# Kernel optimization log

Hardware: AMD Instinct MI355X
Metric: run time of the kernel (lower is better)

The kernel has to match this reference:

```python
import jax, jax.numpy as jnp
import numpy as np

N, F_IN, HEADS, D_HEAD, NCLASS = 4096, 512, 8, 8, 16
NEG_INF = -9e15
LEAKY_SLOPE = 0.2


def setup_inputs() -> dict:
    key = jax.random.key(0)
    ks = jax.random.split(key, 8)
    x = jax.random.normal(ks[0], (N, F_IN), dtype=jnp.float32)
    adj = (jax.random.uniform(ks[1], (N, N)) < 0.01).astype(jnp.float32)
    adj = jnp.maximum(adj, jnp.eye(N, dtype=jnp.float32))
    s1 = 1.0 / np.sqrt(F_IN)
    s2 = 1.0 / np.sqrt(HEADS * D_HEAD)
    W1 = jax.random.normal(ks[2], (HEADS, F_IN, D_HEAD), dtype=jnp.float32) * s1
    a1_src = jax.random.normal(ks[3], (HEADS, D_HEAD), dtype=jnp.float32)
    a1_dst = jax.random.normal(ks[4], (HEADS, D_HEAD), dtype=jnp.float32)
    W2 = jax.random.normal(ks[5], (1, HEADS * D_HEAD, NCLASS), dtype=jnp.float32) * s2
    a2_src = jax.random.normal(ks[6], (1, NCLASS), dtype=jnp.float32)
    a2_dst = jax.random.normal(ks[7], (1, NCLASS), dtype=jnp.float32)
    return {"x": x, "adj": adj, "W1": W1, "a1_src": a1_src, "a1_dst": a1_dst,
            "W2": W2, "a2_src": a2_src, "a2_dst": a2_dst}


def gat_conv(x, adj, W, a_src, a_dst):
    # x: [N, F]; W: [H, F, D]; a_src/a_dst: [H, D]
    h = jnp.einsum('nf,hfd->hnd', x, W)              # [H, N, D]
    e_src = jnp.einsum('hnd,hd->hn', h, a_src)        # [H, N]
    e_dst = jnp.einsum('hnd,hd->hn', h, a_dst)        # [H, N]
    e = e_src[:, :, None] + e_dst[:, None, :]         # [H, N, N]
    e = jax.nn.leaky_relu(e, LEAKY_SLOPE)
    e = jnp.where(adj[None] > 0, e, NEG_INF)
    att = jax.nn.softmax(e, axis=-1)                  # masked row softmax
    out = jnp.einsum('hnm,hmd->hnd', att, h)          # [H, N, D]
    H, n, d = out.shape
    return jnp.transpose(out, (1, 0, 2)).reshape(n, H * d)  # concat heads


def reference(x, adj, W1, a1_src, a1_dst, W2, a2_src, a2_dst):
    # eval mode: dropout is identity
    h = gat_conv(x, adj, W1, a1_src, a1_dst)          # [N, 64]
    h = jax.nn.elu(h)
    out = gat_conv(h, adj, W2, a2_src, a2_dst)        # [N, NCLASS]
    return jax.nn.log_softmax(out, axis=-1)
```

## Files before the change

### kernel.cpp

```cpp
#include <hip/hip_runtime.h>
#include <math.h>

#define NN 4096
#define F_IN 512
#define HEADS 8
#define D_HEAD 8
#define C1 64
#define NCLASS 16
#define MAX_DEG 128
#define LEAKY 0.2f

__global__ __launch_bounds__(256) void k_proj1(const float* __restrict__ x,
                                               const float* __restrict__ W1,
                                               const float* __restrict__ a1s,
                                               const float* __restrict__ a1d,
                                               float* __restrict__ h1,
                                               float* __restrict__ es1,
                                               float* __restrict__ ed1) {
    __shared__ float xs[16 * 512];
    const int t = threadIdx.x;
    const int n0 = blockIdx.x * 16;
    const float4* x4 = (const float4*)(x + (size_t)n0 * F_IN);
    float4* xs4 = (float4*)xs;
#pragma unroll
    for (int i = 0; i < 8; i++) xs4[t + i * 256] = x4[t + i * 256];
    __syncthreads();

    const int c = t & 63;
    const int h = c >> 3, d = c & 7;
    const int rr = t >> 6;
    const float* wp = W1 + h * (F_IN * D_HEAD) + d;
    const float* xr0 = xs + (rr * 4 + 0) * F_IN;
    const float* xr1 = xs + (rr * 4 + 1) * F_IN;
    const float* xr2 = xs + (rr * 4 + 2) * F_IN;
    const float* xr3 = xs + (rr * 4 + 3) * F_IN;
    float a0 = 0.f, a1 = 0.f, a2 = 0.f, a3 = 0.f;
#pragma unroll 8
    for (int f = 0; f < F_IN; f++) {
        float w = wp[f * 8];
        a0 += xr0[f] * w;
        a1 += xr1[f] * w;
        a2 += xr2[f] * w;
        a3 += xr3[f] * w;
    }
    const float as = a1s[c], ad = a1d[c];
    float accs[4] = {a0, a1, a2, a3};
#pragma unroll
    for (int q = 0; q < 4; q++) {
        int n = n0 + rr * 4 + q;
        float v = accs[q];
        h1[(size_t)n * C1 + c] = v;
        float vs = v * as, vd = v * ad;
        vs += __shfl_xor(vs, 1, 64); vd += __shfl_xor(vd, 1, 64);
        vs += __shfl_xor(vs, 2, 64); vd += __shfl_xor(vd, 2, 64);
        vs += __shfl_xor(vs, 4, 64); vd += __shfl_xor(vd, 4, 64);
        if (d == 0) { es1[n * HEADS + h] = vs; ed1[n * HEADS + h] = vd; }
    }
}

__global__ __launch_bounds__(256) void k_csr(const float* __restrict__ adj,
                                             int* __restrict__ deg,
                                             int* __restrict__ cols) {
    __shared__ int cnt;
    __shared__ int cls[MAX_DEG];
    const int n = blockIdx.x, t = threadIdx.x;
    if (t == 0) cnt = 0;
    __syncthreads();
    const float4* row4 = (const float4*)(adj + (size_t)n * NN);
#pragma unroll
    for (int i = 0; i < 4; i++) {
        float4 v = row4[i * 256 + t];
        int base = (i * 256 + t) * 4;
        if (v.x > 0.f) { int p = atomicAdd(&cnt, 1); if (p < MAX_DEG) cls[p] = base; }
        if (v.y > 0.f) { int p = atomicAdd(&cnt, 1); if (p < MAX_DEG) cls[p] = base + 1; }
        if (v.z > 0.f) { int p = atomicAdd(&cnt, 1); if (p < MAX_DEG) cls[p] = base + 2; }
        if (v.w > 0.f) { int p = atomicAdd(&cnt, 1); if (p < MAX_DEG) cls[p] = base + 3; }
    }
    __syncthreads();
    int dc = cnt < MAX_DEG ? cnt : MAX_DEG;
    if (t == 0) deg[n] = dc;
    for (int i = t; i < dc; i += 256) cols[n * MAX_DEG + i] = cls[i];
}

__global__ __launch_bounds__(64) void k_layer1(const float* __restrict__ h1,
                                               const float* __restrict__ es1,
                                               const float* __restrict__ ed1,
                                               const int* __restrict__ deg,
                                               const int* __restrict__ cols,
                                               const float* __restrict__ W2,
                                               const float* __restrict__ a2s,
                                               const float* __restrict__ a2d,
                                               float* __restrict__ h2,
                                               float* __restrict__ es2,
                                               float* __restrict__ ed2) {
    __shared__ int cls[MAX_DEG];
    __shared__ float row[C1];
    const int n = blockIdx.x, t = threadIdx.x;
    const int dg = deg[n];
    for (int i = t; i < dg; i += 64) cls[i] = cols[n * MAX_DEG + i];
    __syncthreads();
    const int h = t >> 3;
    const float es = es1[n * HEADS + h];
    float M = -1e30f, S = 0.f, acc = 0.f;
    int m = cls[0];
    float edv = ed1[m * HEADS + h];
    float hv = h1[(size_t)m * C1 + t];
    for (int j = 0; j < dg; j++) {
        float edc = edv, hvc = hv;
        if (j + 1 < dg) {
            int m2 = cls[j + 1];
            edv = ed1[m2 * HEADS + h];
            hv = h1[(size_t)m2 * C1 + t];
        }
        float e = es + edc;
        e = e > 0.f ? e : LEAKY * e;
        float Mn = fmaxf(M, e);
        float sc = __expf(M - Mn);
        float p = __expf(e - Mn);
        acc = acc * sc + p * hvc;
        S = S * sc + p;
        M = Mn;
    }
    float o = acc / S;
    o = o > 0.f ? o : __expf(o) - 1.f;
    row[t] = o;
    __syncthreads();
    const int k = t & 15, g = t >> 4;
    float hk = 0.f;
#pragma unroll
    for (int cc = 0; cc < 16; cc++) {
        int c = g * 16 + cc;
        hk += row[c] * W2[c * NCLASS + k];
    }
    hk += __shfl_xor(hk, 16, 64);
    hk += __shfl_xor(hk, 32, 64);
    if (t < 16) h2[n * NCLASS + k] = hk;
    float vs = hk * a2s[k];
    float vd = hk * a2d[k];
#pragma unroll
    for (int msk = 8; msk >= 1; msk >>= 1) {
        vs += __shfl_xor(vs, msk, 64);
        vd += __shfl_xor(vd, msk, 64);
    }
    if (t == 0) { es2[n] = vs; ed2[n] = vd; }
}

__global__ __launch_bounds__(64) void k_layer2(const float* __restrict__ h2,
                                               const float* __restrict__ es2,
                                               const float* __restrict__ ed2,
                                               const int* __restrict__ deg,
                                               const int* __restrict__ cols,
                                               float* __restrict__ out) {
    __shared__ int cls[MAX_DEG];
    const int n = blockIdx.x, t = threadIdx.x;
    const int dg = deg[n];
    for (int i = t; i < dg; i += 64) cls[i] = cols[n * MAX_DEG + i];
    __syncthreads();
    const int k = t & 15, g = t >> 4;
    const float es = es2[n];
    float M = -1e30f, S = 0.f, acc = 0.f;
    for (int j = g; j < dg; j += 4) {
        int m = cls[j];
        float e = es + ed2[m];
        e = e > 0.f ? e : LEAKY * e;
        float hv = h2[m * NCLASS + k];
        float Mn = fmaxf(M, e);
        float sc = __expf(M - Mn);
        float p = __expf(e - Mn);
        acc = acc * sc + p * hv;
        S = S * sc + p;
        M = Mn;
    }
#pragma unroll
    for (int msk = 16; msk <= 32; msk <<= 1) {
        float Mo = __shfl_xor(M, msk, 64);
        float So = __shfl_xor(S, msk, 64);
        float ao = __shfl_xor(acc, msk, 64);
        float Mn = fmaxf(M, Mo);
        float s1 = __expf(M - Mn), s2 = __expf(Mo - Mn);
        acc = acc * s1 + ao * s2;
        S = S * s1 + So * s2;
        M = Mn;
    }
    float v = acc / S;
    float mx = v;
#pragma unroll
    for (int msk = 1; msk <= 8; msk <<= 1) mx = fmaxf(mx, __shfl_xor(mx, msk, 64));
    float ex = __expf(v - mx);
    float se = ex;
#pragma unroll
    for (int msk = 1; msk <= 8; msk <<= 1) se += __shfl_xor(se, msk, 64);
    float r = v - mx - __logf(se);
    if (t < 16) out[n * NCLASS + k] = r;
}

extern "C" void kernel_launch(void* const* d_in, const int* in_sizes, int n_in,
                              void* d_out, int out_size, void* d_ws, size_t ws_size,
                              hipStream_t stream) {
    const float* x   = (const float*)d_in[0];
    const float* adj = (const float*)d_in[1];
    const float* W1  = (const float*)d_in[2];
    const float* a1s = (const float*)d_in[3];
    const float* a1d = (const float*)d_in[4];
    const float* W2  = (const float*)d_in[5];
    const float* a2s = (const float*)d_in[6];
    const float* a2d = (const float*)d_in[7];
    float* out = (float*)d_out;

    float* ws  = (float*)d_ws;
    float* h1  = ws;
    float* es1 = h1 + NN * C1;
    float* ed1 = es1 + NN * HEADS;
    float* h2  = ed1 + NN * HEADS;
    float* es2 = h2 + NN * NCLASS;
    float* ed2 = es2 + NN;
    int* deg  = (int*)(ed2 + NN);
    int* cols = deg + NN;

    k_proj1<<<NN / 16, 256, 0, stream>>>(x, W1, a1s, a1d, h1, es1, ed1);
    k_csr<<<NN, 256, 0, stream>>>(adj, deg, cols);
    k_layer1<<<NN, 64, 0, stream>>>(h1, es1, ed1, deg, cols, W2, a2s, a2d, h2, es2, ed2);
    k_layer2<<<NN, 64, 0, stream>>>(h2, es2, ed2, deg, cols, out);
}
```

Baseline: 152.5 us.

## Transpose W1 for vectorized projection and split layer1 aggregation across four waves

A new kernel transposes W1 so each output channel reads a contiguous weight row with float4 loads. The projection now uses 8-row tiles, giving each block 2 rows per wave instead of 4 and twice as many blocks. Layer-1 attention aggregation spreads neighbors over four waves per node and merges the online-softmax partials through shared memory, which adds parallelism but also a merge step and an extra kernel launch.

```diff
diff --git a/kernel.cpp b/kernel.cpp
--- a/kernel.cpp
+++ b/kernel.cpp
@@ -10,45 +10,58 @@
 #define MAX_DEG 128
 #define LEAKY 0.2f
 
+__global__ __launch_bounds__(256) void k_wt(const float* __restrict__ W1,
+                                            float* __restrict__ Wt) {
+    const int i = blockIdx.x * 256 + threadIdx.x;
+#pragma unroll
+    for (int r = 0; r < 4; r++) {
+        int o = r * 8192 + i;
+        int c = o >> 9, f = o & 511;
+        int h = c >> 3, d = c & 7;
+        Wt[o] = W1[(h << 12) | (f << 3) | d];
+    }
+}
+
 __global__ __launch_bounds__(256) void k_proj1(const float* __restrict__ x,
-                                               const float* __restrict__ W1,
+                                               const float* __restrict__ Wt,
                                                const float* __restrict__ a1s,
                                                const float* __restrict__ a1d,
                                                float* __restrict__ h1,
                                                float* __restrict__ es1,
                                                float* __restrict__ ed1) {
-    __shared__ float xs[16 * 512];
+    __shared__ float xs[8 * F_IN];
     const int t = threadIdx.x;
-    const int n0 = blockIdx.x * 16;
+    const int n0 = blockIdx.x * 8;
     const float4* x4 = (const float4*)(x + (size_t)n0 * F_IN);
     float4* xs4 = (float4*)xs;
 #pragma unroll
-    for (int i = 0; i < 8; i++) xs4[t + i * 256] = x4[t + i * 256];
+    for (int i = 0; i < 4; i++) xs4[t + i * 256] = x4[t + i * 256];
     __syncthreads();
 
     const int c = t & 63;
+    const int wv = t >> 6;
+    const float4* wrow = (const float4*)(Wt + c * F_IN);
+    const float4* r0 = (const float4*)(xs + (2 * wv + 0) * F_IN);
+    const float4* r1 = (const float4*)(xs + (2 * wv + 1) * F_IN);
+    float ax0 = 0.f, ay0 = 0.f, az0 = 0.f, aw0 = 0.f;
+    float ax1 = 0.f, ay1 = 0.f, az1 = 0.f, aw1 = 0.f;
+#pragma unroll 4
+    for (int q = 0; q < F_IN / 4; q++) {
+        float4 w = wrow[q];
+        float4 u = r0[q];
+        float4 v = r1[q];
+        ax0 += u.x * w.x; ay0 += u.y * w.y; az0 += u.z * w.z; aw0 += u.w * w.w;
+        ax1 += v.x * w.x; ay1 += v.y * w.y; az1 += v.z * w.z; aw1 += v.w * w.w;
+    }
+    float A = (ax0 + ay0) + (az0 + aw0);
+    float B = (ax1 + ay1) + (az1 + aw1);
+    const float as = a1s[c], ad = a1d[c];
     const int h = c >> 3, d = c & 7;
-    const int rr = t >> 6;
-    const float* wp = W1 + h * (F_IN * D_HEAD) + d;
-    const float* xr0 = xs + (rr * 4 + 0) * F_IN;
-    const float* xr1 = xs + (rr * 4 + 1) * F_IN;
-    const float* xr2 = xs + (rr * 4 + 2) * F_IN;
-    const float* xr3 = xs + (rr * 4 + 3) * F_IN;
-    float a0 = 0.f, a1 = 0.f, a2 = 0.f, a3 = 0.f;
-#pragma unroll 8
-    for (int f = 0; f < F_IN; f++) {
-        float w = wp[f * 8];
-        a0 += xr0[f] * w;
-        a1 += xr1[f] * w;
-        a2 += xr2[f] * w;
-        a3 += xr3[f] * w;
-    }
-    const float as = a1s[c], ad = a1d[c];
-    float accs[4] = {a0, a1, a2, a3};
-#pragma unroll
-    for (int q = 0; q < 4; q++) {
-        int n = n0 + rr * 4 + q;
-        float v = accs[q];
+    float vals[2] = {A, B};
+#pragma unroll
+    for (int q = 0; q < 2; q++) {
+        int n = n0 + 2 * wv + q;
+        float v = vals[q];
         h1[(size_t)n * C1 + c] = v;
         float vs = v * as, vd = v * ad;
         vs += __shfl_xor(vs, 1, 64); vd += __shfl_xor(vd, 1, 64);
@@ -82,67 +95,77 @@
     for (int i = t; i < dc; i += 256) cols[n * MAX_DEG + i] = cls[i];
 }
 
-__global__ __launch_bounds__(64) void k_layer1(const float* __restrict__ h1,
-                                               const float* __restrict__ es1,
-                                               const float* __restrict__ ed1,
-                                               const int* __restrict__ deg,
-                                               const int* __restrict__ cols,
-                                               const float* __restrict__ W2,
-                                               const float* __restrict__ a2s,
-                                               const float* __restrict__ a2d,
-                                               float* __restrict__ h2,
-                                               float* __restrict__ es2,
-                                               float* __restrict__ ed2) {
+__global__ __launch_bounds__(256) void k_layer1(const float* __restrict__ h1,
+                                                const float* __restrict__ es1,
+                                                const float* __restrict__ ed1,
+                                                const int* __restrict__ deg,
+                                                const int* __restrict__ cols,
+                                                const float* __restrict__ W2,
+                                                const float* __restrict__ a2s,
+                                                const float* __restrict__ a2d,
+                                                float* __restrict__ h2,
+                                                float* __restrict__ es2,
+                                                float* __restrict__ ed2) {
     __shared__ int cls[MAX_DEG];
+    __shared__ float pM[4][C1], pS[4][C1], pA[4][C1];
     __shared__ float row[C1];
     const int n = blockIdx.x, t = threadIdx.x;
+    const int wv = t >> 6, ln = t & 63;
     const int dg = deg[n];
-    for (int i = t; i < dg; i += 64) cls[i] = cols[n * MAX_DEG + i];
-    __syncthreads();
-    const int h = t >> 3;
+    for (int i = t; i < dg; i += 256) cls[i] = cols[n * MAX_DEG + i];
+    __syncthreads();
+    const int h = ln >> 3;
     const float es = es1[n * HEADS + h];
     float M = -1e30f, S = 0.f, acc = 0.f;
-    int m = cls[0];
-    float edv = ed1[m * HEADS + h];
-    float hv = h1[(size_t)m * C1 + t];
-    for (int j = 0; j < dg; j++) {
-        float edc = edv, hvc = hv;
-        if (j + 1 < dg) {
-            int m2 = cls[j + 1];
-            edv = ed1[m2 * HEADS + h];
-            hv = h1[(size_t)m2 * C1 + t];
-        }
-        float e = es + edc;
+    for (int j = wv; j < dg; j += 4) {
+        int m = cls[j];
+        float e = es + ed1[m * HEADS + h];
         e = e > 0.f ? e : LEAKY * e;
+        float hv = h1[(size_t)m * C1 + ln];
         float Mn = fmaxf(M, e);
         float sc = __expf(M - Mn);
         float p = __expf(e - Mn);
-        acc = acc * sc + p * hvc;
+        acc = acc * sc + p * hv;
         S = S * sc + p;
         M = Mn;
     }
-    float o = acc / S;
-    o = o > 0.f ? o : __expf(o) - 1.f;
-    row[t] = o;
-    __syncthreads();
-    const int k = t & 15, g = t >> 4;
-    float hk = 0.f;
-#pragma unroll
-    for (int cc = 0; cc < 16; cc++) {
-        int c = g * 16 + cc;
-        hk += row[c] * W2[c * NCLASS + k];
-    }
-    hk += __shfl_xor(hk, 16, 64);
-    hk += __shfl_xor(hk, 32, 64);
-    if (t < 16) h2[n * NCLASS + k] = hk;
-    float vs = hk * a2s[k];
-    float vd = hk * a2d[k];
-#pragma unroll
-    for (int msk = 8; msk >= 1; msk >>= 1) {
-        vs += __shfl_xor(vs, msk, 64);
-        vd += __shfl_xor(vd, msk, 64);
-    }
-    if (t == 0) { es2[n] = vs; ed2[n] = vd; }
+    pM[wv][ln] = M; pS[wv][ln] = S; pA[wv][ln] = acc;
+    __syncthreads();
+    if (wv == 0) {
+#pragma unroll
+        for (int q = 1; q < 4; q++) {
+            float Mo = pM[q][ln], So = pS[q][ln], ao = pA[q][ln];
+            float Mn = fmaxf(M, Mo);
+            float s1 = __expf(M - Mn), s2 = __expf(Mo - Mn);
+            acc = acc * s1 + ao * s2;
+            S = S * s1 + So * s2;
+            M = Mn;
+        }
+        float o = acc / S;
+        o = o > 0.f ? o : __expf(o) - 1.f;
+        row[ln] = o;
+    }
+    __syncthreads();
+    if (wv == 0) {
+        const int k = ln & 15, g = ln >> 4;
+        float hk = 0.f;
+#pragma unroll
+        for (int cc = 0; cc < 16; cc++) {
+            int c2 = g * 16 + cc;
+            hk += row[c2] * W2[c2 * NCLASS + k];
+        }
+        hk += __shfl_xor(hk, 16, 64);
+        hk += __shfl_xor(hk, 32, 64);
+        if (ln < 16) h2[n * NCLASS + k] = hk;
+        float vs = hk * a2s[k];
+        float vd = hk * a2d[k];
+#pragma unroll
+        for (int msk = 8; msk >= 1; msk >>= 1) {
+            vs += __shfl_xor(vs, msk, 64);
+            vd += __shfl_xor(vd, msk, 64);
+        }
+        if (ln == 0) { es2[n] = vs; ed2[n] = vd; }
+    }
 }
 
 __global__ __launch_bounds__(64) void k_layer2(const float* __restrict__ h2,
@@ -216,9 +239,11 @@
     float* ed2 = es2 + NN;
     int* deg  = (int*)(ed2 + NN);
     int* cols = deg + NN;
-
-    k_proj1<<<NN / 16, 256, 0, stream>>>(x, W1, a1s, a1d, h1, es1, ed1);
+    float* Wt = (float*)(cols + NN * MAX_DEG);
+
+    k_wt<<<32, 256, 0, stream>>>(W1, Wt);
     k_csr<<<NN, 256, 0, stream>>>(adj, deg, cols);
-    k_layer1<<<NN, 64, 0, stream>>>(h1, es1, ed1, deg, cols, W2, a2s, a2d, h2, es2, ed2);
+    k_proj1<<<NN / 8, 256, 0, stream>>>(x, Wt, a1s, a1d, h1, es1, ed1);
+    k_layer1<<<NN, 256, 0, stream>>>(h1, es1, ed1, deg, cols, W2, a2s, a2d, h2, es2, ed2);
     k_layer2<<<NN, 64, 0, stream>>>(h2, es2, ed2, deg, cols, out);
 }
```

Result: slower. 161.8 us (+6.1%).
